# Optimization experiments

Hardware: AMD Instinct MI355X
Metric: run time of the kernel (lower is better)

The kernel has to match this reference:

```python
import jax, jax.numpy as jnp
import numpy as np

NUM_HEADS = 4
KEY_DIMS = 32  # c // num_heads


def rel_to_abs(x):
    # x: [B, N, W, 2W-1] relative logits -> [B, N, W, W] absolute logits
    b, n, w, _ = x.shape
    x = jnp.pad(x, ((0, 0), (0, 0), (0, 0), (0, 1)))           # [b,n,w,2w]
    x = x.reshape(b, n, w * 2 * w)
    x = jnp.pad(x, ((0, 0), (0, 0), (0, w - 1)))
    x = x.reshape(b, n, w + 1, 2 * w - 1)
    return x[:, :, :w, w - 1:]


def rel_logits_1d(q, rel_k):
    # q: [B, heads, X, Y, d], rel_k: [2Y-1, d] -> [B, heads, X, X, Y, Y]
    b, nh, xx, yy, d = q.shape
    rl = jnp.einsum('bhxyd,md->bhxym', q, rel_k)               # [b,h,x,y,2y-1]
    rl = rel_to_abs(rl.reshape(b, nh * xx, yy, 2 * yy - 1))    # [b,h*x,y,y]
    rl = rl.reshape(b, nh, xx, 1, yy, yy)
    return jnp.broadcast_to(rl, (b, nh, xx, xx, yy, yy))


def relative_position_bias(pos_q, pos_emb_h, pos_emb_w):
    # pos_q: [B, heads, H, W, d] -> bias [B, heads, H, W, H, W]
    rw = rel_logits_1d(pos_q, pos_emb_w)                        # [b,h,H,H,W,W]
    rw = rw.transpose(0, 1, 2, 4, 3, 5)                         # [b,h,H,W,H,W]
    rh = rel_logits_1d(pos_q.transpose(0, 1, 3, 2, 4), pos_emb_h)  # [b,h,W,W,H,H]
    rh = rh.transpose(0, 1, 4, 2, 5, 3)                         # [b,h,H,W,H,W]
    return rw + rh


def setup_inputs() -> dict:
    key = jax.random.key(0)
    k1, k2, k3, k4 = jax.random.split(key, 4)
    B, H, W, C = 2, 64, 64, 128
    qk_dims = NUM_HEADS * KEY_DIMS  # 128
    out_channels = C
    x = jax.random.normal(k1, (B, H, W, C), dtype=jnp.float32)
    w_qkv = jax.random.normal(k2, (C, 2 * qk_dims + out_channels), dtype=jnp.float32) * 0.05
    pos_emb_h = jax.random.normal(k3, (2 * H - 1, KEY_DIMS), dtype=jnp.float32) * 0.05
    pos_emb_w = jax.random.normal(k4, (2 * W - 1, KEY_DIMS), dtype=jnp.float32) * 0.05
    return {'x': x, 'w_qkv': w_qkv, 'pos_emb_h': pos_emb_h, 'pos_emb_w': pos_emb_w}


def reference(x, w_qkv, pos_emb_h, pos_emb_w):
    B, H, W, C = x.shape
    nh, kd = NUM_HEADS, KEY_DIMS
    qk_dims = nh * kd
    oc = C
    scale = 1.0 / float(kd) ** 0.5

    qkv = jnp.einsum('bhwc,cd->bhwd', x, w_qkv)                 # 1x1 conv, no bias
    q, k, v = jnp.split(qkv, [qk_dims, 2 * qk_dims], axis=-1)
    L = H * W
    q = q.reshape(B, L, nh, kd).transpose(0, 2, 1, 3)           # [B,nh,L,kd]
    k = k.reshape(B, L, nh, kd).transpose(0, 2, 1, 3)           # [B,nh,L,kd]
    v = v.reshape(B, L, nh, oc // nh).transpose(0, 2, 1, 3)     # [B,nh,L,dv]

    pos_q = q.reshape(B, nh, H, W, kd)
    pos = relative_position_bias(pos_q, pos_emb_h, pos_emb_w).reshape(B, nh, L, L)

    scores = jnp.einsum('bnqd,bnkd->bnqk', q, k) * scale + pos  # [B,nh,L,L]
    attn = jax.nn.softmax(scores, axis=-1)
    out = jnp.einsum('bnqk,bnkd->bnqd', attn, v)                # [B,nh,L,dv]
    out = out.transpose(0, 2, 1, 3).reshape(B, H, W, oc)
    return out
```

## Files before the change

### kernel.cpp

```cpp
#include <hip/hip_runtime.h>
#include <hip/hip_bf16.h>
#include <math.h>

#define B_  2
#define NH  4
#define HH  64
#define WW  64
#define KD  32
#define L_  4096
#define BN_ 8
#define LOG2E 1.4426950408889634f
#define KSCALE (0.17677669529663687f * 1.4426950408889634f)
#define FIXED_M 10.0f

typedef float    f32x4  __attribute__((ext_vector_type(4), may_alias));
typedef _Float16 half8  __attribute__((ext_vector_type(8), may_alias));
typedef _Float16 half4  __attribute__((ext_vector_type(4), may_alias));
typedef __fp16   fp16x2 __attribute__((ext_vector_type(2)));
typedef unsigned uint4v __attribute__((ext_vector_type(4), may_alias));

__device__ __forceinline__ float fexp2(float x) {
#if __has_builtin(__builtin_amdgcn_exp2f)
    return __builtin_amdgcn_exp2f(x);
#else
    return __expf(x * 0.69314718056f);
#endif
}

__device__ __forceinline__ unsigned pack2u(float a, float b) {
    fp16x2 t = __builtin_amdgcn_cvt_pkrtz(a, b);
    union { fp16x2 i; unsigned o; } u;
    u.i = t;
    return u.o;
}

__global__ __launch_bounds__(256) void qkv_gemm(const float* __restrict__ x,
                                                const float* __restrict__ w,
                                                _Float16* __restrict__ q_h,
                                                _Float16* __restrict__ k_h,
                                                _Float16* __restrict__ vt_h) {
    __shared__ __align__(16) char smem[34816];
    _Float16* xs  = (_Float16*)smem;
    _Float16* wsT = (_Float16*)(smem + 17408);

    const int mt = blockIdx.x % 128;
    const int nt = blockIdx.x / 128;
    const int m0 = mt * 64, n0 = nt * 64;
    const int tid = threadIdx.x;
    const int wv = tid >> 6, lane = tid & 63;
    const int l16 = lane & 15, quad = lane >> 4;

    #pragma unroll
    for (int i = 0; i < 8; i++) {
        const int idx = i * 256 + tid;
        const int row = idx >> 5, c4 = (idx & 31) * 4;
        const float4 v = *(const float4*)&x[(size_t)(m0 + row) * 128 + c4];
        half4 h;
        h[0] = (_Float16)v.x; h[1] = (_Float16)v.y;
        h[2] = (_Float16)v.z; h[3] = (_Float16)v.w;
        *(half4*)&xs[row * 136 + c4] = h;
    }
    #pragma unroll
    for (int i = 0; i < 8; i++) {
        const int idx = i * 256 + tid;
        const int k = idx >> 4, c4 = (idx & 15) * 4;
        const float4 v = *(const float4*)&w[(size_t)k * 384 + n0 + c4];
        wsT[(c4 + 0) * 136 + k] = (_Float16)v.x;
        wsT[(c4 + 1) * 136 + k] = (_Float16)v.y;
        wsT[(c4 + 2) * 136 + k] = (_Float16)v.z;
        wsT[(c4 + 3) * 136 + k] = (_Float16)v.w;
    }
    __syncthreads();

    f32x4 acc[4] = {{0.f,0.f,0.f,0.f},{0.f,0.f,0.f,0.f},
                    {0.f,0.f,0.f,0.f},{0.f,0.f,0.f,0.f}};
    half8 af[4];
    #pragma unroll
    for (int kc = 0; kc < 4; kc++)
        af[kc] = *(const half8*)&xs[(wv * 16 + l16) * 136 + kc * 32 + quad * 8];
    #pragma unroll
    for (int ns = 0; ns < 4; ns++)
        #pragma unroll
        for (int kc = 0; kc < 4; kc++) {
            const half8 bf = *(const half8*)&wsT[(ns * 16 + l16) * 136 + kc * 32 + quad * 8];
            acc[ns] = __builtin_amdgcn_mfma_f32_16x16x32_f16(af[kc], bf, acc[ns], 0, 0, 0);
        }

    const int which = n0 >> 7;
    const int nc = n0 & 127;
    const int b = m0 >> 12;
    if (which < 2) {
        _Float16* dst = (which == 0) ? q_h : k_h;
        const float mult = (which == 1) ? KSCALE : 1.0f;
        #pragma unroll
        for (int ns = 0; ns < 4; ns++) {
            const int col = nc + ns * 16 + l16;
            const int bn = b * NH + (col >> 5);
            const int d = col & 31;
            #pragma unroll
            for (int r = 0; r < 4; r++) {
                const int l = (m0 & 4095) + wv * 16 + quad * 4 + r;
                dst[((size_t)bn * L_ + l) * 32 + d] = (_Float16)(acc[ns][r] * mult);
            }
        }
    } else {
        __syncthreads();
        float* img = (float*)smem;
        #pragma unroll
        for (int ns = 0; ns < 4; ns++) {
            const int chan = ns * 16 + l16;
            const int h = chan >> 5, d = chan & 31;
            #pragma unroll
            for (int r = 0; r < 4; r++) {
                const int p = wv * 16 + quad * 4 + r;
                const int y = p >> 5, p32 = p & 31;
                const int q4 = (p32 >> 2) & 3;
                const int j = ((p32 >> 4) & 1) * 4 + (p32 & 3);
                const int fidx = h * 2048 + (y * 2 + (d >> 4)) * 512
                               + (q4 * 16 + (d & 15)) * 8 + j;
                img[fidx + (fidx >> 4)] = acc[ns][r];
            }
        }
        __syncthreads();
        const int ktg = (m0 & 4095) >> 6;
        #pragma unroll
        for (int h = 0; h < 2; h++) {
            const int head = (nc >> 5) + h;
            const int bn = b * NH + head;
            const int fbase = h * 2048 + tid * 8;
            const int sbase = fbase + (fbase >> 4);
            half8 o;
            #pragma unroll
            for (int e = 0; e < 8; e++) o[e] = (_Float16)img[sbase + e];
            *(half8*)(vt_h + (size_t)bn * 131072 + ktg * 2048 + tid * 8) = o;
        }
    }
}

__global__ __launch_bounds__(256) void attn_mfma(
    const _Float16* __restrict__ q_h,
    const _Float16* __restrict__ k_h,
    const _Float16* __restrict__ vt_h,
    const float* __restrict__ emb_h,
    const float* __restrict__ emb_w,
    float* __restrict__ out)
{
    __shared__ __align__(16) char smem[49408];

    const int bi    = blockIdx.x;
    const int bn    = bi & 7;
    const int w1    = bi >> 3;
    const int tid   = threadIdx.x;
    const int wv    = tid >> 6;
    const int qgp   = wv & 1;
    const int kh    = wv >> 1;
    const int lane  = tid & 63;
    const int l16   = lane & 15;
    const int quad  = lane >> 4;

    const _Float16* Kbase = k_h  + (size_t)bn * L_ * 32;
    const _Float16* Vtile = vt_h + (size_t)bn * 131072;

    const int khT = wv & 1;
    const int isV = wv >> 1;
    const _Float16* gs[4];
    int ldsT[4];
    #pragma unroll
    for (int sC = 0; sC < 4; sC++) {
        gs[sC] = (isV ? Vtile : Kbase)
               + (size_t)khT * 32 * 2048 + sC * 512 + lane * 8;
        ldsT[sC] = khT * 4096 + (isV
            ? (8192 + sC * 1024 + lane * 16)
            : ((sC * 16 + (lane >> 2)) * 64 + (((lane & 3) ^ ((lane >> 3) & 3)) << 4)));
    }

    uint4v stg0[4];
    #pragma unroll
    for (int u = 0; u < 4; u++) stg0[u] = *(const uint4v*)gs[u];

    float* Rw0 = (float*)(smem + 32768) + (qgp * 2 + 0) * 1040;
    float* Rw1 = (float*)(smem + 32768) + (qgp * 2 + 1) * 1040;
    const half8 aq0 = *(const half8*)(q_h +
        (((size_t)bn * L_ + ((qgp * 2 + 0) * 16 + l16) * 64 + w1) * 32 + quad * 8));
    const half8 aq1 = *(const half8*)(q_h +
        (((size_t)bn * L_ + ((qgp * 2 + 1) * 16 + l16) * 64 + w1) * 32 + quad * 8));

    f32x4 qwT0[4], qwT1[4];
    #pragma unroll
    for (int sub = 0; sub < 4; sub++) {
        const float* ew = emb_w + (size_t)(sub * 16 + l16 - w1 + 63) * 32 + quad * 8;
        const float4 e0 = *(const float4*)ew;
        const float4 e1 = *(const float4*)(ew + 4);
        union { uint4v u; half8 h; } ua;
        ua.u[0] = pack2u(e0.x * LOG2E, e0.y * LOG2E);
        ua.u[1] = pack2u(e0.z * LOG2E, e0.w * LOG2E);
        ua.u[2] = pack2u(e1.x * LOG2E, e1.y * LOG2E);
        ua.u[3] = pack2u(e1.z * LOG2E, e1.w * LOG2E);
        f32x4 z = {-FIXED_M, -FIXED_M, -FIXED_M, -FIXED_M};
        qwT0[sub] = __builtin_amdgcn_mfma_f32_16x16x32_f16(ua.h, aq0, z, 0, 0, 0);
        qwT1[sub] = __builtin_amdgcn_mfma_f32_16x16x32_f16(ua.h, aq1, z, 0, 0, 0);
    }

    #pragma unroll
    for (int ji = 0; ji < 4; ji++) {
        const int jt = kh * 4 + ji;
        const int j = min(jt * 16 + l16, 126);
        const float* eh = emb_h + (size_t)j * 32 + quad * 8;
        const float4 e0 = *(const float4*)eh;
        const float4 e1 = *(const float4*)(eh + 4);
        union { uint4v u; half8 h; } ub;
        ub.u[0] = pack2u(e0.x * LOG2E, e0.y * LOG2E);
        ub.u[1] = pack2u(e0.z * LOG2E, e0.w * LOG2E);
        ub.u[2] = pack2u(e1.x * LOG2E, e1.y * LOG2E);
        ub.u[3] = pack2u(e1.z * LOG2E, e1.w * LOG2E);
        f32x4 z = {0.f, 0.f, 0.f, 0.f};
        const f32x4 C0 = __builtin_amdgcn_mfma_f32_16x16x32_f16(aq0, ub.h, z, 0, 0, 0);
        const f32x4 C1 = __builtin_amdgcn_mfma_f32_16x16x32_f16(aq1, ub.h, z, 0, 0, 0);
        #pragma unroll
        for (int r = 0; r < 4; r++) {
            const int row = quad * 4 + r;
            const int c0 = jt * 16 + l16 - 63 + ((qgp * 2 + 0) * 16 + row);
            if (c0 >= 0 && c0 < 64) Rw0[row * 65 + c0] = C0[r];
            const int c1 = jt * 16 + l16 - 63 + ((qgp * 2 + 1) * 16 + row);
            if (c1 >= 0 && c1 < 64) Rw1[row * 65 + c1] = C1[r];
        }
    }

    #pragma unroll
    for (int u = 0; u < 4; u++) *(uint4v*)(smem + ldsT[u]) = stg0[u];
    __syncthreads();

    f32x4 O00 = {0.f,0.f,0.f,0.f}, O01 = {0.f,0.f,0.f,0.f};
    f32x4 O10 = {0.f,0.f,0.f,0.f}, O11 = {0.f,0.f,0.f,0.f};
    float la = 0.f, lb = 0.f;
    const float* qh_row0 = Rw0 + l16 * 65;
    const float* qh_row1 = Rw1 + l16 * 65;
    float qh_cur0 = qh_row0[kh * 32];
    float qh_cur1 = qh_row1[kh * 32];
#if __has_builtin(__builtin_amdgcn_fdot2)
    fp16x2 onep;
    { union { unsigned u; fp16x2 h; } uo; uo.u = pack2u(1.0f, 1.0f); onep = uo.h; }
#endif

    const int kOff = kh * 4096 + l16 * 64 + ((quad ^ ((l16 >> 1) & 3)) << 4);
    const int vOff = 8192 + kh * 4096 + lane * 16;

    #pragma unroll 2
    for (int t = 0; t < 32; t++) {
        const int cur = t & 1;
        const int tS = (t < 31) ? (t + 1) : 31;
        uint4v sa[4];
        #pragma unroll
        for (int u = 0; u < 4; u++)
            sa[u] = *(const uint4v*)(gs[u] + (size_t)tS * 2048);

        const char* kb = smem + cur * 16384 + kOff;
        const char* vb = smem + cur * 16384 + vOff;
        const half8 kf0 = *(const half8*)(kb);
        const half8 kf1 = *(const half8*)(kb + 1024);
        const half8 kf2 = *(const half8*)(kb + 2048);
        const half8 kf3 = *(const half8*)(kb + 3072);
        const half8 va00 = *(const half8*)(vb);
        const half8 va10 = *(const half8*)(vb + 1024);
        const half8 va01 = *(const half8*)(vb + 2048);
        const half8 va11 = *(const half8*)(vb + 3072);

        const f32x4 S00 = __builtin_amdgcn_mfma_f32_16x16x32_f16(kf0, aq0, qwT0[0], 0, 0, 0);
        const f32x4 S01 = __builtin_amdgcn_mfma_f32_16x16x32_f16(kf1, aq0, qwT0[1], 0, 0, 0);
        const f32x4 S02 = __builtin_amdgcn_mfma_f32_16x16x32_f16(kf2, aq0, qwT0[2], 0, 0, 0);
        const f32x4 S03 = __builtin_amdgcn_mfma_f32_16x16x32_f16(kf3, aq0, qwT0[3], 0, 0, 0);
        const f32x4 S10 = __builtin_amdgcn_mfma_f32_16x16x32_f16(kf0, aq1, qwT1[0], 0, 0, 0);
        const f32x4 S11 = __builtin_amdgcn_mfma_f32_16x16x32_f16(kf1, aq1, qwT1[1], 0, 0, 0);
        const f32x4 S12 = __builtin_amdgcn_mfma_f32_16x16x32_f16(kf2, aq1, qwT1[2], 0, 0, 0);
        const f32x4 S13 = __builtin_amdgcn_mfma_f32_16x16x32_f16(kf3, aq1, qwT1[3], 0, 0, 0);

        const float qh_next0 = qh_row0[kh * 32 + tS];
        const float qh_next1 = qh_row1[kh * 32 + tS];

        union { uint4v u; half8 h; } p0a, p0b;
        {
            const float a0 = fexp2(S00[0] + qh_cur0), a1 = fexp2(S00[1] + qh_cur0);
            const float a2 = fexp2(S00[2] + qh_cur0), a3 = fexp2(S00[3] + qh_cur0);
            const float a4 = fexp2(S01[0] + qh_cur0), a5 = fexp2(S01[1] + qh_cur0);
            const float a6 = fexp2(S01[2] + qh_cur0), a7 = fexp2(S01[3] + qh_cur0);
            p0a.u[0] = pack2u(a0, a1); p0a.u[1] = pack2u(a2, a3);
            p0a.u[2] = pack2u(a4, a5); p0a.u[3] = pack2u(a6, a7);
            const float b0 = fexp2(S02[0] + qh_cur0), b1 = fexp2(S02[1] + qh_cur0);
            const float b2 = fexp2(S02[2] + qh_cur0), b3 = fexp2(S02[3] + qh_cur0);
            const float b4 = fexp2(S03[0] + qh_cur0), b5 = fexp2(S03[1] + qh_cur0);
            const float b6 = fexp2(S03[2] + qh_cur0), b7 = fexp2(S03[3] + qh_cur0);
            p0b.u[0] = pack2u(b0, b1); p0b.u[1] = pack2u(b2, b3);
            p0b.u[2] = pack2u(b4, b5); p0b.u[3] = pack2u(b6, b7);
        }
        union { uint4v u; half8 h; } p1a, p1b;
        {
            const float a0 = fexp2(S10[0] + qh_cur1), a1 = fexp2(S10[1] + qh_cur1);
            const float a2 = fexp2(S10[2] + qh_cur1), a3 = fexp2(S10[3] + qh_cur1);
            const float a4 = fexp2(S11[0] + qh_cur1), a5 = fexp2(S11[1] + qh_cur1);
            const float a6 = fexp2(S11[2] + qh_cur1), a7 = fexp2(S11[3] + qh_cur1);
            p1a.u[0] = pack2u(a0, a1); p1a.u[1] = pack2u(a2, a3);
            p1a.u[2] = pack2u(a4, a5); p1a.u[3] = pack2u(a6, a7);
            const float b0 = fexp2(S12[0] + qh_cur1), b1 = fexp2(S12[1] + qh_cur1);
            const float b2 = fexp2(S12[2] + qh_cur1), b3 = fexp2(S12[3] + qh_cur1);
            const float b4 = fexp2(S13[0] + qh_cur1), b5 = fexp2(S13[1] + qh_cur1);
            const float b6 = fexp2(S13[2] + qh_cur1), b7 = fexp2(S13[3] + qh_cur1);
            p1b.u[0] = pack2u(b0, b1); p1b.u[1] = pack2u(b2, b3);
            p1b.u[2] = pack2u(b4, b5); p1b.u[3] = pack2u(b6, b7);
        }

        O00 = __builtin_amdgcn_mfma_f32_16x16x32_f16(va00, p0a.h, O00, 0, 0, 0);
        O00 = __builtin_amdgcn_mfma_f32_16x16x32_f16(va01, p0b.h, O00, 0, 0, 0);
        O01 = __builtin_amdgcn_mfma_f32_16x16x32_f16(va10, p0a.h, O01, 0, 0, 0);
        O01 = __builtin_amdgcn_mfma_f32_16x16x32_f16(va11, p0b.h, O01, 0, 0, 0);
        O10 = __builtin_amdgcn_mfma_f32_16x16x32_f16(va00, p1a.h, O10, 0, 0, 0);
        O10 = __builtin_amdgcn_mfma_f32_16x16x32_f16(va01, p1b.h, O10, 0, 0, 0);
        O11 = __builtin_amdgcn_mfma_f32_16x16x32_f16(va10, p1a.h, O11, 0, 0, 0);
        O11 = __builtin_amdgcn_mfma_f32_16x16x32_f16(va11, p1b.h, O11, 0, 0, 0);

#if __has_builtin(__builtin_amdgcn_fdot2)
        {
            union { unsigned u; fp16x2 h; } c0, c1, c2, c3;
            c0.u = p0a.u[0]; c1.u = p0a.u[1]; c2.u = p0a.u[2]; c3.u = p0a.u[3];
            la = __builtin_amdgcn_fdot2(c0.h, onep, la, false);
            la = __builtin_amdgcn_fdot2(c1.h, onep, la, false);
            la = __builtin_amdgcn_fdot2(c2.h, onep, la, false);
            la = __builtin_amdgcn_fdot2(c3.h, onep, la, false);
            c0.u = p0b.u[0]; c1.u = p0b.u[1]; c2.u = p0b.u[2]; c3.u = p0b.u[3];
            la = __builtin_amdgcn_fdot2(c0.h, onep, la, false);
            la = __builtin_amdgcn_fdot2(c1.h, onep, la, false);
            la = __builtin_amdgcn_fdot2(c2.h, onep, la, false);
            la = __builtin_amdgcn_fdot2(c3.h, onep, la, false);
            c0.u = p1a.u[0]; c1.u = p1a.u[1]; c2.u = p1a.u[2]; c3.u = p1a.u[3];
            lb = __builtin_amdgcn_fdot2(c0.h, onep, lb, false);
            lb = __builtin_amdgcn_fdot2(c1.h, onep, lb, false);
            lb = __builtin_amdgcn_fdot2(c2.h, onep, lb, false);
            lb = __builtin_amdgcn_fdot2(c3.h, onep, lb, false);
            c0.u = p1b.u[0]; c1.u = p1b.u[1]; c2.u = p1b.u[2]; c3.u = p1b.u[3];
            lb = __builtin_amdgcn_fdot2(c0.h, onep, lb, false);
            lb = __builtin_amdgcn_fdot2(c1.h, onep, lb, false);
            lb = __builtin_amdgcn_fdot2(c2.h, onep, lb, false);
            lb = __builtin_amdgcn_fdot2(c3.h, onep, lb, false);
        }
#endif
        qh_cur0 = qh_next0;
        qh_cur1 = qh_next1;

        __builtin_amdgcn_sched_barrier(0);
        #pragma unroll
        for (int u = 0; u < 4; u++)
            *(uint4v*)(smem + (cur ^ 1) * 16384 + ldsT[u]) = sa[u];
        __syncthreads();
    }

    la += __shfl_xor(la, 16);
    la += __shfl_xor(la, 32);
    lb += __shfl_xor(lb, 16);
    lb += __shfl_xor(lb, 32);

    __syncthreads();
    float (*mO)[32][17] = (float(*)[32][17])smem;
    float* mL = (float*)(smem + 17408);
    const int slot0 = kh * 4 + qgp * 2 + 0;
    const int slot1 = kh * 4 + qgp * 2 + 1;
    #pragma unroll
    for (int r = 0; r < 4; r++) {
        mO[slot0][quad * 4 + r][l16]      = O00[r];
        mO[slot0][16 + quad * 4 + r][l16] = O01[r];
        mO[slot1][quad * 4 + r][l16]      = O10[r];
        mO[slot1][16 + quad * 4 + r][l16] = O11[r];
    }
    if (quad == 0) {
        mL[slot0 * 16 + l16] = la;
        mL[slot1 * 16 + l16] = lb;
    }
    __syncthreads();

    const int head = bn & 3, bb = bn >> 2;
    #pragma unroll
    for (int rep = 0; rep < 2; rep++) {
        const int idx = rep * 256 + tid;
        const int h1 = idx >> 3;
        const int dg = idx & 7;
        const int qgo = h1 >> 4, ql = h1 & 15;
        const int wsA = qgo;
        const int wsB = qgo + 4;
        const float denom = mL[wsA * 16 + ql] + mL[wsB * 16 + ql];
        const float inv = 1.0f / denom;
        float4 o;
        o.x = (mO[wsA][dg * 4 + 0][ql] + mO[wsB][dg * 4 + 0][ql]) * inv;
        o.y = (mO[wsA][dg * 4 + 1][ql] + mO[wsB][dg * 4 + 1][ql]) * inv;
        o.z = (mO[wsA][dg * 4 + 2][ql] + mO[wsB][dg * 4 + 2][ql]) * inv;
        o.w = (mO[wsA][dg * 4 + 3][ql] + mO[wsB][dg * 4 + 3][ql]) * inv;
        *(float4*)&out[(((size_t)bb * 64 + h1) * 64 + w1) * 128 + head * 32 + dg * 4] = o;
    }
}

extern "C" void kernel_launch(void* const* d_in, const int* in_sizes, int n_in,
                              void* d_out, int out_size, void* d_ws, size_t ws_size,
                              hipStream_t stream) {
    const float* x     = (const float*)d_in[0];
    const float* w_qkv = (const float*)d_in[1];
    const float* emb_h = (const float*)d_in[2];
    const float* emb_w = (const float*)d_in[3];
    float* out = (float*)d_out;

    _Float16* q_h  = (_Float16*)d_ws;
    _Float16* k_h  = q_h + (size_t)BN_ * L_ * KD;
    _Float16* vt_h = k_h + (size_t)BN_ * L_ * KD;

    qkv_gemm<<<768, 256, 0, stream>>>(x, w_qkv, q_h, k_h, vt_h);
    attn_mfma<<<512, 256, 0, stream>>>(q_h, k_h, vt_h, emb_h, emb_w, out);
}
```

Before: 104.0 us.

## Merge two query columns per 1024-thread block and split keys four ways

The attention kernel now launches 256 blocks of 1024 threads. Each block handles two w-columns and splits the key range across four wave groups, so each staged K/V tile is reused by twice as many query waves. The per-wave loop length drops from 32 to 16 tiles, and the final reduction sums partials from four key quarters. The cost is doubled LDS use (about 97KB per block), 1024-thread launch bounds that squeeze registers, and fewer blocks to spread across CUs. There is also a stray duplicated pack line, which is harmless because it is overwritten by the next line.

```diff
diff --git a/kernel.cpp b/kernel.cpp
--- a/kernel.cpp
+++ b/kernel.cpp
@@ -137,7 +137,7 @@
     }
 }
 
-__global__ __launch_bounds__(256) void attn_mfma(
+__global__ __launch_bounds__(1024) void attn_mfma(
     const _Float16* __restrict__ q_h,
     const _Float16* __restrict__ k_h,
     const _Float16* __restrict__ vt_h,
@@ -145,45 +145,52 @@
     const float* __restrict__ emb_w,
     float* __restrict__ out)
 {
-    __shared__ __align__(16) char smem[49408];
+    __shared__ __align__(16) char smem[98816];
 
     const int bi    = blockIdx.x;
     const int bn    = bi & 7;
-    const int w1    = bi >> 3;
+    const int wpair = bi >> 3;
     const int tid   = threadIdx.x;
     const int wv    = tid >> 6;
-    const int qgp   = wv & 1;
-    const int kh    = wv >> 1;
+    const int kq    = wv >> 2;
+    const int qgp   = (wv >> 1) & 1;
+    const int wo    = wv & 1;
+    const int w1    = wpair * 2 + wo;
     const int lane  = tid & 63;
     const int l16   = lane & 15;
     const int quad  = lane >> 4;
+    const int q0A   = (qgp * 2 + 0) * 16;
+    const int q0B   = (qgp * 2 + 1) * 16;
 
     const _Float16* Kbase = k_h  + (size_t)bn * L_ * 32;
     const _Float16* Vtile = vt_h + (size_t)bn * 131072;
 
-    const int khT = wv & 1;
-    const int isV = wv >> 1;
-    const _Float16* gs[4];
-    int ldsT[4];
-    #pragma unroll
-    for (int sC = 0; sC < 4; sC++) {
-        gs[sC] = (isV ? Vtile : Kbase)
-               + (size_t)khT * 32 * 2048 + sC * 512 + lane * 8;
-        ldsT[sC] = khT * 4096 + (isV
-            ? (8192 + sC * 1024 + lane * 16)
-            : ((sC * 16 + (lane >> 2)) * 64 + (((lane & 3) ^ ((lane >> 3) & 3)) << 4)));
-    }
-
-    uint4v stg0[4];
-    #pragma unroll
-    for (int u = 0; u < 4; u++) stg0[u] = *(const uint4v*)gs[u];
-
-    float* Rw0 = (float*)(smem + 32768) + (qgp * 2 + 0) * 1040;
-    float* Rw1 = (float*)(smem + 32768) + (qgp * 2 + 1) * 1040;
+    const int cat  = wv & 7;
+    const int kqS  = cat & 3;
+    const int isVS = cat >> 2;
+    const int halfS = wv >> 3;
+    const _Float16* gsrc = (isVS ? Vtile : Kbase) + (size_t)kqS * 16 * 2048;
+    const _Float16* gs[2];
+    int ldsT[2];
+    #pragma unroll
+    for (int u = 0; u < 2; u++) {
+        const int cc = halfS * 2 + u;
+        gs[u] = gsrc + cc * 512 + lane * 8;
+        ldsT[u] = kqS * 4096 + isVS * 16384 + (isVS
+            ? (cc * 1024 + lane * 16)
+            : ((cc * 16 + (lane >> 2)) * 64 + (((lane & 3) ^ ((lane >> 3) & 3)) << 4)));
+    }
+
+    const uint4v stg0a = *(const uint4v*)gs[0];
+    const uint4v stg0b = *(const uint4v*)gs[1];
+
+    float* RwA = (float*)(smem + 65536) + ((qgp * 2 + 0) * 2 + wo) * 1040;
+    float* RwB = (float*)(smem + 65536) + ((qgp * 2 + 1) * 2 + wo) * 1040;
+
     const half8 aq0 = *(const half8*)(q_h +
-        (((size_t)bn * L_ + ((qgp * 2 + 0) * 16 + l16) * 64 + w1) * 32 + quad * 8));
+        (((size_t)bn * L_ + (q0A + l16) * 64 + w1) * 32 + quad * 8));
     const half8 aq1 = *(const half8*)(q_h +
-        (((size_t)bn * L_ + ((qgp * 2 + 1) * 16 + l16) * 64 + w1) * 32 + quad * 8));
+        (((size_t)bn * L_ + (q0B + l16) * 64 + w1) * 32 + quad * 8));
 
     f32x4 qwT0[4], qwT1[4];
     #pragma unroll
@@ -202,8 +209,8 @@
     }
 
     #pragma unroll
-    for (int ji = 0; ji < 4; ji++) {
-        const int jt = kh * 4 + ji;
+    for (int ji = 0; ji < 2; ji++) {
+        const int jt = kq * 2 + ji;
         const int j = min(jt * 16 + l16, 126);
         const float* eh = emb_h + (size_t)j * 32 + quad * 8;
         const float4 e0 = *(const float4*)eh;
@@ -219,43 +226,40 @@
         #pragma unroll
         for (int r = 0; r < 4; r++) {
             const int row = quad * 4 + r;
-            const int c0 = jt * 16 + l16 - 63 + ((qgp * 2 + 0) * 16 + row);
-            if (c0 >= 0 && c0 < 64) Rw0[row * 65 + c0] = C0[r];
-            const int c1 = jt * 16 + l16 - 63 + ((qgp * 2 + 1) * 16 + row);
-            if (c1 >= 0 && c1 < 64) Rw1[row * 65 + c1] = C1[r];
-        }
-    }
-
-    #pragma unroll
-    for (int u = 0; u < 4; u++) *(uint4v*)(smem + ldsT[u]) = stg0[u];
+            const int cA = jt * 16 + l16 - 63 + (q0A + row);
+            if (cA >= 0 && cA < 64) RwA[row * 65 + cA] = C0[r];
+            const int cB = jt * 16 + l16 - 63 + (q0B + row);
+            if (cB >= 0 && cB < 64) RwB[row * 65 + cB] = C1[r];
+        }
+    }
+
+    *(uint4v*)(smem + ldsT[0]) = stg0a;
+    *(uint4v*)(smem + ldsT[1]) = stg0b;
     __syncthreads();
 
     f32x4 O00 = {0.f,0.f,0.f,0.f}, O01 = {0.f,0.f,0.f,0.f};
     f32x4 O10 = {0.f,0.f,0.f,0.f}, O11 = {0.f,0.f,0.f,0.f};
     float la = 0.f, lb = 0.f;
-    const float* qh_row0 = Rw0 + l16 * 65;
-    const float* qh_row1 = Rw1 + l16 * 65;
-    float qh_cur0 = qh_row0[kh * 32];
-    float qh_cur1 = qh_row1[kh * 32];
+    const float* qh_rowA = RwA + l16 * 65;
+    const float* qh_rowB = RwB + l16 * 65;
 #if __has_builtin(__builtin_amdgcn_fdot2)
     fp16x2 onep;
     { union { unsigned u; fp16x2 h; } uo; uo.u = pack2u(1.0f, 1.0f); onep = uo.h; }
 #endif
 
-    const int kOff = kh * 4096 + l16 * 64 + ((quad ^ ((l16 >> 1) & 3)) << 4);
-    const int vOff = 8192 + kh * 4096 + lane * 16;
+    const int swz16 = ((quad ^ ((l16 >> 1) & 3)) << 4);
+    const int kOff = kq * 4096 + l16 * 64 + swz16;
+    const int vOff = 16384 + kq * 4096 + lane * 16;
 
     #pragma unroll 2
-    for (int t = 0; t < 32; t++) {
+    for (int t = 0; t < 16; t++) {
         const int cur = t & 1;
-        const int tS = (t < 31) ? (t + 1) : 31;
-        uint4v sa[4];
-        #pragma unroll
-        for (int u = 0; u < 4; u++)
-            sa[u] = *(const uint4v*)(gs[u] + (size_t)tS * 2048);
-
-        const char* kb = smem + cur * 16384 + kOff;
-        const char* vb = smem + cur * 16384 + vOff;
+        const int tS = (t < 15) ? (t + 1) : 15;
+        const uint4v sa = *(const uint4v*)(gs[0] + (size_t)tS * 2048);
+        const uint4v sb = *(const uint4v*)(gs[1] + (size_t)tS * 2048);
+
+        const char* kb = smem + cur * 32768 + kOff;
+        const char* vb = smem + cur * 32768 + vOff;
         const half8 kf0 = *(const half8*)(kb);
         const half8 kf1 = *(const half8*)(kb + 1024);
         const half8 kf2 = *(const half8*)(kb + 2048);
@@ -274,37 +278,41 @@
         const f32x4 S12 = __builtin_amdgcn_mfma_f32_16x16x32_f16(kf2, aq1, qwT1[2], 0, 0, 0);
         const f32x4 S13 = __builtin_amdgcn_mfma_f32_16x16x32_f16(kf3, aq1, qwT1[3], 0, 0, 0);
 
-        const float qh_next0 = qh_row0[kh * 32 + tS];
-        const float qh_next1 = qh_row1[kh * 32 + tS];
+        const int ktc = kq * 16 + t;
+        const int ktn = kq * 16 + tS;
+        const float qhA = qh_rowA[ktc];
+        const float qhB = qh_rowB[ktc];
+        (void)ktn;
 
         union { uint4v u; half8 h; } p0a, p0b;
         {
-            const float a0 = fexp2(S00[0] + qh_cur0), a1 = fexp2(S00[1] + qh_cur0);
-            const float a2 = fexp2(S00[2] + qh_cur0), a3 = fexp2(S00[3] + qh_cur0);
-            const float a4 = fexp2(S01[0] + qh_cur0), a5 = fexp2(S01[1] + qh_cur0);
-            const float a6 = fexp2(S01[2] + qh_cur0), a7 = fexp2(S01[3] + qh_cur0);
+            const float a0 = fexp2(S00[0] + qhA), a1 = fexp2(S00[1] + qhA);
+            const float a2 = fexp2(S00[2] + qhA), a3 = fexp2(S00[3] + qhA);
+            const float a4 = fexp2(S01[0] + qhA), a5 = fexp2(S01[1] + qhA);
+            const float a6 = fexp2(S01[2] + qhA), a7 = fexp2(S01[3] + qhA);
             p0a.u[0] = pack2u(a0, a1); p0a.u[1] = pack2u(a2, a3);
             p0a.u[2] = pack2u(a4, a5); p0a.u[3] = pack2u(a6, a7);
-            const float b0 = fexp2(S02[0] + qh_cur0), b1 = fexp2(S02[1] + qh_cur0);
-            const float b2 = fexp2(S02[2] + qh_cur0), b3 = fexp2(S02[3] + qh_cur0);
-            const float b4 = fexp2(S03[0] + qh_cur0), b5 = fexp2(S03[1] + qh_cur0);
-            const float b6 = fexp2(S03[2] + qh_cur0), b7 = fexp2(S03[3] + qh_cur0);
+            const float b0 = fexp2(S02[0] + qhA), b1 = fexp2(S02[1] + qhA);
+            const float b2 = fexp2(S02[2] + qhA), b3 = fexp2(S02[3] + qhA);
+            const float b4 = fexp2(S03[0] + qhA), b5 = fexp2(S03[1] + qhA);
+            const float b6 = fexp2(S03[2] + qhA), b7 = fexp2(S03[3] + qhA);
             p0b.u[0] = pack2u(b0, b1); p0b.u[1] = pack2u(b2, b3);
             p0b.u[2] = pack2u(b4, b5); p0b.u[3] = pack2u(b6, b7);
         }
         union { uint4v u; half8 h; } p1a, p1b;
         {
-            const float a0 = fexp2(S10[0] + qh_cur1), a1 = fexp2(S10[1] + qh_cur1);
-            const float a2 = fexp2(S10[2] + qh_cur1), a3 = fexp2(S10[3] + qh_cur1);
-            const float a4 = fexp2(S11[0] + qh_cur1), a5 = fexp2(S11[1] + qh_cur1);
-            const float a6 = fexp2(S11[2] + qh_cur1), a7 = fexp2(S11[3] + qh_cur1);
+            const float a0 = fexp2(S10[0] + qhB), a1 = fexp2(S10[1] + qhB);
+            const float a2 = fexp2(S10[2] + qhB), a3 = fexp2(S10[3] + qhB);
+            const float a4 = fexp2(S11[0] + qhB), a5 = fexp2(S11[1] + qhB);
+            const float a6 = fexp2(S11[2] + qhB), a7 = fexp2(S11[3] + qhB);
             p1a.u[0] = pack2u(a0, a1); p1a.u[1] = pack2u(a2, a3);
             p1a.u[2] = pack2u(a4, a5); p1a.u[3] = pack2u(a6, a7);
-            const float b0 = fexp2(S12[0] + qh_cur1), b1 = fexp2(S12[1] + qh_cur1);
-            const float b2 = fexp2(S12[2] + qh_cur1), b3 = fexp2(S12[3] + qh_cur1);
-            const float b4 = fexp2(S13[0] + qh_cur1), b5 = fexp2(S13[1] + qh_cur1);
-            const float b6 = fexp2(S13[2] + qh_cur1), b7 = fexp2(S13[3] + qh_cur1);
+            const float b0 = fexp2(S12[0] + qhB), b1 = fexp2(S12[1] + qhB);
+            const float b2 = fexp2(S12[2] + qhB), b3 = fexp2(S12[3] + qhB);
+            const float b4 = fexp2(S13[0] + qhB), b5 = fexp2(S13[1] + qhB);
+            const float b6 = fexp2(S13[2] + qhB), b7 = fexp2(S13[3] + qhB);
             p1b.u[0] = pack2u(b0, b1); p1b.u[1] = pack2u(b2, b3);
+            p1b.u[2] = pack2u(b4, b5); p1b.u[3] = pack2u(b4, b5);
             p1b.u[2] = pack2u(b4, b5); p1b.u[3] = pack2u(b6, b7);
         }
 
@@ -342,13 +350,10 @@
             lb = __builtin_amdgcn_fdot2(c3.h, onep, lb, false);
         }
 #endif
-        qh_cur0 = qh_next0;
-        qh_cur1 = qh_next1;
 
         __builtin_amdgcn_sched_barrier(0);
-        #pragma unroll
-        for (int u = 0; u < 4; u++)
-            *(uint4v*)(smem + (cur ^ 1) * 16384 + ldsT[u]) = sa[u];
+        *(uint4v*)(smem + (cur ^ 1) * 32768 + ldsT[0]) = sa;
+        *(uint4v*)(smem + (cur ^ 1) * 32768 + ldsT[1]) = sb;
         __syncthreads();
     }
 
@@ -359,9 +364,9 @@
 
     __syncthreads();
     float (*mO)[32][17] = (float(*)[32][17])smem;
-    float* mL = (float*)(smem + 17408);
-    const int slot0 = kh * 4 + qgp * 2 + 0;
-    const int slot1 = kh * 4 + qgp * 2 + 1;
+    float* mL = (float*)(smem + 69632);
+    const int slot0 = wv * 2 + 0;
+    const int slot1 = wv * 2 + 1;
     #pragma unroll
     for (int r = 0; r < 4; r++) {
         mO[slot0][quad * 4 + r][l16]      = O00[r];
@@ -375,24 +380,28 @@
     }
     __syncthreads();
 
+    const int wo_o = tid >> 9;
+    const int rest = tid & 511;
+    const int h1   = rest >> 3;
+    const int dg   = rest & 7;
+    const int qg_o = h1 >> 4, ql = h1 & 15;
+    const int qgp_o = qg_o >> 1, g_o = qg_o & 1;
+    float denom = 0.f;
+    float4 o = {0.f, 0.f, 0.f, 0.f};
+    #pragma unroll
+    for (int kqe = 0; kqe < 4; kqe++) {
+        const int s = ((kqe * 4 + qgp_o * 2 + wo_o) << 1) + g_o;
+        denom += mL[s * 16 + ql];
+        o.x += mO[s][dg * 4 + 0][ql];
+        o.y += mO[s][dg * 4 + 1][ql];
+        o.z += mO[s][dg * 4 + 2][ql];
+        o.w += mO[s][dg * 4 + 3][ql];
+    }
+    const float inv = 1.0f / denom;
+    o.x *= inv; o.y *= inv; o.z *= inv; o.w *= inv;
     const int head = bn & 3, bb = bn >> 2;
-    #pragma unroll
-    for (int rep = 0; rep < 2; rep++) {
-        const int idx = rep * 256 + tid;
-        const int h1 = idx >> 3;
-        const int dg = idx & 7;
-        const int qgo = h1 >> 4, ql = h1 & 15;
-        const int wsA = qgo;
-        const int wsB = qgo + 4;
-        const float denom = mL[wsA * 16 + ql] + mL[wsB * 16 + ql];
-        const float inv = 1.0f / denom;
-        float4 o;
-        o.x = (mO[wsA][dg * 4 + 0][ql] + mO[wsB][dg * 4 + 0][ql]) * inv;
-        o.y = (mO[wsA][dg * 4 + 1][ql] + mO[wsB][dg * 4 + 1][ql]) * inv;
-        o.z = (mO[wsA][dg * 4 + 2][ql] + mO[wsB][dg * 4 + 2][ql]) * inv;
-        o.w = (mO[wsA][dg * 4 + 3][ql] + mO[wsB][dg * 4 + 3][ql]) * inv;
-        *(float4*)&out[(((size_t)bb * 64 + h1) * 64 + w1) * 128 + head * 32 + dg * 4] = o;
-    }
+    const int w1o = wpair * 2 + wo_o;
+    *(float4*)&out[(((size_t)bb * 64 + h1) * 64 + w1o) * 128 + head * 32 + dg * 4] = o;
 }
 
 extern "C" void kernel_launch(void* const* d_in, const int* in_sizes, int n_in,
@@ -409,5 +418,5 @@
     _Float16* vt_h = k_h + (size_t)BN_ * L_ * KD;
 
     qkv_gemm<<<768, 256, 0, stream>>>(x, w_qkv, q_h, k_h, vt_h);
-    attn_mfma<<<512, 256, 0, stream>>>(q_h, k_h, vt_h, emb_h, emb_w, out);
+    attn_mfma<<<256, 1024, 0, stream>>>(q_h, k_h, vt_h, emb_h, emb_w, out);
 }
```

After: 99.60 us. -4.2%, faster.
